# Optimization experiments

Hardware: AMD Instinct MI355X
Metric: run time of the kernel (lower is better)

Reference implementation:

```python
import jax, jax.numpy as jnp
import numpy as np

B, N, D, S, ITERS, EPS = 32, 4096, 512, 8, 3, 1e-8


def layer_norm(x, g, b, eps=1e-5):
    mu = jnp.mean(x, axis=-1, keepdims=True)
    var = jnp.var(x, axis=-1, keepdims=True)
    return (x - mu) * jax.lax.rsqrt(var + eps) * g + b


def setup_inputs() -> dict:
    key = jax.random.key(0)
    ks = jax.random.split(key, 12)
    sc = 1.0 / np.sqrt(D)
    return {
        "inputs": jax.random.normal(ks[0], (B, N, D), jnp.float32),
        "noise": jax.random.normal(ks[1], (B, S, D), jnp.float32),
        "slots_mu": jax.random.normal(ks[2], (1, S, D), jnp.float32),
        "slots_sigma": jnp.ones((1, S, D), jnp.float32),
        "ln_in_g": jnp.ones((D,), jnp.float32), "ln_in_b": jnp.zeros((D,), jnp.float32),
        "ln_s_g": jnp.ones((D,), jnp.float32), "ln_s_b": jnp.zeros((D,), jnp.float32),
        "wq": jax.random.normal(ks[3], (D, D), jnp.float32) * sc,
        "wk": jax.random.normal(ks[4], (D, D), jnp.float32) * sc,
        "wv": jax.random.normal(ks[5], (D, D), jnp.float32) * sc,
        "w_ih": jax.random.normal(ks[6], (3 * D, D), jnp.float32) * sc,
        "w_hh": jax.random.normal(ks[7], (3 * D, D), jnp.float32) * sc,
        "b_ih": jnp.zeros((3 * D,), jnp.float32),
        "b_hh": jnp.zeros((3 * D,), jnp.float32),
        "ln_m_g": jnp.ones((D,), jnp.float32), "ln_m_b": jnp.zeros((D,), jnp.float32),
        "w1": jax.random.normal(ks[8], (D, D), jnp.float32) * sc,
        "b1": jnp.zeros((D,), jnp.float32),
        "w2": jax.random.normal(ks[9], (D, D), jnp.float32) * sc,
        "b2": jnp.zeros((D,), jnp.float32),
    }


def reference(inputs, noise, slots_mu, slots_sigma, ln_in_g, ln_in_b, ln_s_g, ln_s_b,
              wq, wk, wv, w_ih, w_hh, b_ih, b_hh, ln_m_g, ln_m_b, w1, b1, w2, b2):
    # slot init: mu + sigma * N(0,1)
    slots = slots_mu + slots_sigma * noise          # (B,S,D)
    x = layer_norm(inputs, ln_in_g, ln_in_b)        # (B,N,D)
    k = jnp.einsum('bnd,ed->bne', x, wk)            # (B,N,D)
    v = jnp.einsum('bnd,ed->bne', x, wv)            # (B,N,D)
    for _ in range(ITERS):
        slots_prev = slots
        sn = layer_norm(slots, ln_s_g, ln_s_b)
        q = jnp.einsum('bsd,ed->bse', sn, wq)       # (B,S,D)
        logits = jnp.einsum('bnd,bsd->bns', k, q)   # (B,N,S)
        attn = jax.nn.softmax(logits, axis=-1) + EPS  # softmax over slots
        attn = attn / jnp.sum(attn, axis=-1, keepdims=True)
        attn_t = jnp.swapaxes(attn, -1, -2)         # (B,S,N)
        updates = jnp.einsum('bsn,bnd->bsd', attn_t, v)
        # GRUCell(input=updates, hidden=slots_prev)
        gi = jnp.einsum('bsd,ed->bse', updates, w_ih) + b_ih
        gh = jnp.einsum('bsd,ed->bse', slots_prev, w_hh) + b_hh
        gi_r, gi_z, gi_n = jnp.split(gi, 3, axis=-1)
        gh_r, gh_z, gh_n = jnp.split(gh, 3, axis=-1)
        r = jax.nn.sigmoid(gi_r + gh_r)
        z = jax.nn.sigmoid(gi_z + gh_z)
        n = jnp.tanh(gi_n + r * gh_n)
        slots = (1.0 - z) * n + z * slots_prev
        # residual MLP
        h = layer_norm(slots, ln_m_g, ln_m_b)
        h = jax.nn.relu(jnp.einsum('bsd,ed->bse', h, w1) + b1)
        slots = slots + jnp.einsum('bsd,ed->bse', h, w2) + b2
    return slots
```

## Files before the change

kernel.cpp:

```cpp
#include <hip/hip_runtime.h>

#define B_ 32
#define N_ 4096
#define D_ 512
#define S_ 8
#define ITERS_ 3

__device__ __forceinline__ float sigmoid_f(float x) {
    return 1.0f / (1.0f + __expf(-x));
}
__device__ __forceinline__ float tanh_f(float x) {
    float e = __expf(2.0f * x);
    return 1.0f - 2.0f / (e + 1.0f);
}

template<int WT, int LNA>
__device__ void gemm_body(const float* __restrict__ A, const float* __restrict__ W,
                          const float* __restrict__ bias, float* __restrict__ C,
                          int M, int N, int K, int bxi, int byi,
                          const float* __restrict__ stats,
                          const float* __restrict__ lng, const float* __restrict__ lnb,
                          float* smem) {
    float (*As)[68] = (float (*)[68])smem;
    float (*Ws)[36] = (float (*)[36])(smem + 64 * 68);
    int t  = threadIdx.x;
    int bm = byi * 64, bn = bxi * 32;
    int tm = t >> 4, tn = t & 15;
    float acc[4][2] = {{0.f,0.f},{0.f,0.f},{0.f,0.f},{0.f,0.f}};

    for (int kk = 0; kk < K; kk += 64) {
        __syncthreads();
        if (WT == 2) {
#pragma unroll
            for (int r = 0; r < 4; ++r) {
                int idx = t + r * 256;
                int k = idx >> 4, m4 = idx & 15;
                float4 a4 = *(const float4*)(A + (size_t)(kk + k) * M + bm + (m4 << 2));
                *(float4*)&As[k][m4 << 2] = a4;
            }
        } else {
#pragma unroll
            for (int r = 0; r < 4; ++r) {
                int flat = t * 4 + r * 1024;
                int m = flat >> 6, k = flat & 63;
                float4 a4 = *(const float4*)(A + (size_t)(bm + m) * K + kk + k);
                if (LNA) {
                    float mean = stats[(bm + m) * 2];
                    float rs   = stats[(bm + m) * 2 + 1];
                    float4 g4 = *(const float4*)(lng + kk + k);
                    float4 b4 = *(const float4*)(lnb + kk + k);
                    a4.x = fmaf((a4.x - mean) * rs, g4.x, b4.x);
                    a4.y = fmaf((a4.y - mean) * rs, g4.y, b4.y);
                    a4.z = fmaf((a4.z - mean) * rs, g4.z, b4.z);
                    a4.w = fmaf((a4.w - mean) * rs, g4.w, b4.w);
                }
                As[k + 0][m] = a4.x; As[k + 1][m] = a4.y;
                As[k + 2][m] = a4.z; As[k + 3][m] = a4.w;
            }
        }
        if (WT == 1) {
#pragma unroll
            for (int r = 0; r < 2; ++r) {
                int flat = t * 4 + r * 1024;
                int n = flat >> 6, k = flat & 63;
                float4 w4 = *(const float4*)(W + (size_t)(bn + n) * K + kk + k);
                Ws[k + 0][n] = w4.x; Ws[k + 1][n] = w4.y;
                Ws[k + 2][n] = w4.z; Ws[k + 3][n] = w4.w;
            }
        } else {
#pragma unroll
            for (int r = 0; r < 2; ++r) {
                int flat = t * 4 + r * 1024;
                int k = flat >> 5, n = flat & 31;
                float4 w4 = *(const float4*)(W + (size_t)(kk + k) * N + bn + n);
                *(float4*)&Ws[k][n] = w4;
            }
        }
        __syncthreads();
#pragma unroll
        for (int k = 0; k < 64; ++k) {
            float4 a = *(const float4*)&As[k][tm << 2];
            float2 w = *(const float2*)&Ws[k][tn << 1];
            acc[0][0] = fmaf(a.x, w.x, acc[0][0]); acc[0][1] = fmaf(a.x, w.y, acc[0][1]);
            acc[1][0] = fmaf(a.y, w.x, acc[1][0]); acc[1][1] = fmaf(a.y, w.y, acc[1][1]);
            acc[2][0] = fmaf(a.z, w.x, acc[2][0]); acc[2][1] = fmaf(a.z, w.y, acc[2][1]);
            acc[3][0] = fmaf(a.w, w.x, acc[3][0]); acc[3][1] = fmaf(a.w, w.y, acc[3][1]);
        }
    }
#pragma unroll
    for (int i = 0; i < 4; ++i) {
#pragma unroll
        for (int j = 0; j < 2; ++j) {
            int row = bm + (tm << 2) + i;
            int col = bn + (tn << 1) + j;
            float v = acc[i][j];
            if (bias) v += bias[col];
            C[(size_t)row * N + col] = v;
        }
    }
}

__device__ void init_body(const float* __restrict__ noise, const float* __restrict__ mu,
                          const float* __restrict__ sg, float* __restrict__ slots,
                          float* __restrict__ stats, int blk) {
    int wid = threadIdx.x >> 6, lane = threadIdx.x & 63;
    int row = blk * 4 + wid;
    const float4* nz = (const float4*)(noise + (size_t)row * D_);
    const float4* m4 = (const float4*)(mu + (size_t)(row & 7) * D_);
    const float4* s4 = (const float4*)(sg + (size_t)(row & 7) * D_);
    float4 v0 = nz[lane], v1 = nz[64 + lane];
    float4 a0 = m4[lane], a1 = m4[64 + lane];
    float4 c0 = s4[lane], c1 = s4[64 + lane];
    v0.x = fmaf(c0.x, v0.x, a0.x); v0.y = fmaf(c0.y, v0.y, a0.y);
    v0.z = fmaf(c0.z, v0.z, a0.z); v0.w = fmaf(c0.w, v0.w, a0.w);
    v1.x = fmaf(c1.x, v1.x, a1.x); v1.y = fmaf(c1.y, v1.y, a1.y);
    v1.z = fmaf(c1.z, v1.z, a1.z); v1.w = fmaf(c1.w, v1.w, a1.w);
    float4* o4 = (float4*)(slots + (size_t)row * D_);
    o4[lane] = v0; o4[64 + lane] = v1;
    float s1 = v0.x + v0.y + v0.z + v0.w + v1.x + v1.y + v1.z + v1.w;
    float s2 = v0.x*v0.x; s2 = fmaf(v0.y,v0.y,s2); s2 = fmaf(v0.z,v0.z,s2); s2 = fmaf(v0.w,v0.w,s2);
    s2 = fmaf(v1.x,v1.x,s2); s2 = fmaf(v1.y,v1.y,s2); s2 = fmaf(v1.z,v1.z,s2); s2 = fmaf(v1.w,v1.w,s2);
#pragma unroll
    for (int off = 32; off > 0; off >>= 1) {
        s1 += __shfl_xor(s1, off, 64);
        s2 += __shfl_xor(s2, off, 64);
    }
    if (lane == 0) {
        float mean = s1 * (1.0f / D_);
        float var  = s2 * (1.0f / D_) - mean * mean;
        stats[row * 2]     = mean;
        stats[row * 2 + 1] = rsqrtf(var + 1e-5f);
    }
}

__global__ __launch_bounds__(256) void k_pro(const float* __restrict__ wk, const float* __restrict__ wq,
                                             const float* __restrict__ w_ih, const float* __restrict__ wv,
                                             float* __restrict__ Mqk, float* __restrict__ Wiv,
                                             const float* __restrict__ noise, const float* __restrict__ mu,
                                             const float* __restrict__ sg, float* __restrict__ slots,
                                             float* __restrict__ stats) {
    __shared__ float smem[64 * 68 + 64 * 36];
    int blk = blockIdx.x;
    if (blk < 128) {
        gemm_body<2,0>(wk, wq, nullptr, Mqk, 512, 512, 512, blk & 15, blk >> 4,
                       nullptr, nullptr, nullptr, smem);
    } else if (blk < 512) {
        int t2 = blk - 128;
        gemm_body<0,0>(w_ih, wv, nullptr, Wiv, 1536, 512, 512, t2 & 15, t2 >> 4,
                       nullptr, nullptr, nullptr, smem);
    } else {
        init_body(noise, mu, sg, slots, stats, blk - 512);
    }
}

template<int WT, int LNA>
__global__ __launch_bounds__(256) void k_gemm(const float* __restrict__ A, const float* __restrict__ W,
                                              const float* __restrict__ bias, float* __restrict__ C,
                                              int M, int N, int K,
                                              const float* __restrict__ stats,
                                              const float* __restrict__ lng, const float* __restrict__ lnb) {
    __shared__ float smem[64 * 68 + 64 * 36];
    gemm_body<WT,LNA>(A, W, bias, C, M, N, K, blockIdx.x, blockIdx.y, stats, lng, lnb, smem);
}

template<int FIRST>
__global__ __launch_bounds__(512, 2) void k_attn_gh(const float* __restrict__ x,
                                                    const float* __restrict__ qk,
                                                    const float* __restrict__ g,
                                                    const float* __restrict__ bvec,
                                                    float* __restrict__ part,
                                                    float* __restrict__ bsum,
                                                    float2* __restrict__ murs,
                                                    const float* __restrict__ slots,
                                                    const float* __restrict__ w_hh,
                                                    const float* __restrict__ b_hh,
                                                    float* __restrict__ gg) {
    __shared__ float smem[8704];
    const int blk = blockIdx.x;
    const int t = threadIdx.x;

    if (blk >= 512) {
        const int t2 = blk - 512;
        const int ci = t2 % 24, ri = t2 / 24;
        const int bm = ri * 64, bn = ci * 64;
        float (*As)[68] = (float (*)[68])smem;
        float (*Ws)[68] = (float (*)[68])(smem + 64 * 68);
        const int tm = t >> 5, tn = t & 31;
        float acc[4][2] = {{0.f,0.f},{0.f,0.f},{0.f,0.f},{0.f,0.f}};
        for (int kk = 0; kk < 512; kk += 64) {
            __syncthreads();
#pragma unroll
            for (int r = 0; r < 2; ++r) {
                int flat = t * 4 + r * 2048;
                int m = flat >> 6, k = flat & 63;
                float4 a4 = *(const float4*)(slots + (size_t)(bm + m) * 512 + kk + k);
                As[k + 0][m] = a4.x; As[k + 1][m] = a4.y;
                As[k + 2][m] = a4.z; As[k + 3][m] = a4.w;
            }
#pragma unroll
            for (int r = 0; r < 2; ++r) {
                int flat = t * 4 + r * 2048;
                int n = flat >> 6, k = flat & 63;
                float4 w4 = *(const float4*)(w_hh + (size_t)(bn + n) * 512 + kk + k);
                Ws[k + 0][n] = w4.x; Ws[k + 1][n] = w4.y;
                Ws[k + 2][n] = w4.z; Ws[k + 3][n] = w4.w;
            }
            __syncthreads();
#pragma unroll
            for (int k = 0; k < 64; ++k) {
                const float4 a = *(const float4*)&As[k][tm << 2];
                const float2 w = *(const float2*)&Ws[k][tn << 1];
                acc[0][0] = fmaf(a.x, w.x, acc[0][0]); acc[0][1] = fmaf(a.x, w.y, acc[0][1]);
                acc[1][0] = fmaf(a.y, w.x, acc[1][0]); acc[1][1] = fmaf(a.y, w.y, acc[1][1]);
                acc[2][0] = fmaf(a.z, w.x, acc[2][0]); acc[2][1] = fmaf(a.z, w.y, acc[2][1]);
                acc[3][0] = fmaf(a.w, w.x, acc[3][0]); acc[3][1] = fmaf(a.w, w.y, acc[3][1]);
            }
        }
#pragma unroll
        for (int i = 0; i < 4; ++i) {
#pragma unroll
            for (int j = 0; j < 2; ++j) {
                int row = bm + (tm << 2) + i;
                int col = bn + (tn << 1) + j;
                gg[(size_t)row * 3072 + col] = acc[i][j] + b_hh[col];
            }
        }
        return;
    }

    float* qts  = smem;
    float* dds  = smem + 4096;
    float* wls  = smem + 4480;
    float* mur  = smem + 4864;
    float* redA = smem + 5376;
    float* redB = smem + 5392;
    float* c12  = smem + 5408;
    float* u0s  = smem;
    const int nc = blk & 15, b = blk >> 4;
    const int w = t >> 6, lane = t & 63;
    const size_t rowbase = (size_t)b * N_ + (size_t)nc * 256;

    {
        const float4* qk4 = (const float4*)(qk + (size_t)b * 4096);
        const float4* g4 = (const float4*)g;
        const float4* b4 = (const float4*)bvec;
        float c1p[2], c2p[2];
#pragma unroll
        for (int r = 0; r < 2; ++r) {
            int f = t + r * 512;
            float4 v = qk4[f];
            float4 gg4 = g4[f & 127];
            float4 bb = b4[f & 127];
            float4 qv = make_float4(v.x*gg4.x, v.y*gg4.y, v.z*gg4.z, v.w*gg4.w);
            *(float4*)&qts[((f & 127) * 8 + (f >> 7)) * 4] = qv;
            c1p[r] = qv.x + qv.y + qv.z + qv.w;
            c2p[r] = bb.x*v.x + bb.y*v.y + bb.z*v.z + bb.w*v.w;
        }
#pragma unroll
        for (int off = 32; off > 0; off >>= 1) {
#pragma unroll
            for (int r = 0; r < 2; ++r) {
                c1p[r] += __shfl_xor(c1p[r], off, 64);
                c2p[r] += __shfl_xor(c2p[r], off, 64);
            }
        }
        if (lane == 0) {
            redA[w * 2 + 0] = c1p[0]; redA[w * 2 + 1] = c1p[1];
            redB[w * 2 + 0] = c2p[0]; redB[w * 2 + 1] = c2p[1];
        }
    }
    if (!FIRST && t < 256) {
        float2 mm = murs[rowbase + t];
        mur[2 * t] = mm.x; mur[2 * t + 1] = mm.y;
    }
    __syncthreads();
    if (t < 8) {
        int s = t;
        float v1, v2;
        if (s < 4) { v1 = redA[4*s]       + redA[4*s + 2];     v2 = redB[4*s]       + redB[4*s + 2]; }
        else       { v1 = redA[4*(s-4)+1] + redA[4*(s-4)+3];   v2 = redB[4*(s-4)+1] + redB[4*(s-4)+3]; }
        c12[s] = v1; c12[8 + s] = v2;
    }
    __syncthreads();

    float4 qa[8], qb[8];
#pragma unroll
    for (int s = 0; s < 8; ++s) {
        qa[s] = *(const float4*)&qts[(lane * 8 + s) * 4];
        qb[s] = *(const float4*)&qts[((64 + lane) * 8 + s) * 4];
    }
    float c1r[8], c2r[8];
#pragma unroll
    for (int s = 0; s < 8; ++s) { c1r[s] = c12[s]; c2r[s] = c12[8 + s]; }

    const bool hb5 = (lane & 32) != 0, hb4 = (lane & 16) != 0, hb3 = (lane & 8) != 0;
    const float cnorm = 1.0f / (1.0f + 8.0f * 1e-8f);
    const float eadd  = 1e-8f * cnorm;

    float4 acc0[8], acc1[8];
#pragma unroll
    for (int s = 0; s < 8; ++s) {
        acc0[s] = make_float4(0.f, 0.f, 0.f, 0.f);
        acc1[s] = make_float4(0.f, 0.f, 0.f, 0.f);
    }
    float aS8[8] = {0,0,0,0,0,0,0,0}, tS8[8] = {0,0,0,0,0,0,0,0};

    const float4* xg = (const float4*)(x + rowbase * D_);
    float4 cur[8], nxt[8];
    {
        int r0 = w * 4;
#pragma unroll
        for (int i = 0; i < 4; ++i) {
            cur[2*i]   = xg[(size_t)(r0 + i) * 128 + lane];
            cur[2*i+1] = xg[(size_t)(r0 + i) * 128 + 64 + lane];
        }
    }

    for (int jb = 0; jb < 8; ++jb) {
#pragma unroll
        for (int i = 0; i < 4; ++i) {
            float4 xa = cur[2*i], xb = cur[2*i+1];
            float dd[8];
#pragma unroll
            for (int s = 0; s < 8; ++s) {
                float td = xa.x * qa[s].x;
                td = fmaf(xa.y, qa[s].y, td); td = fmaf(xa.z, qa[s].z, td); td = fmaf(xa.w, qa[s].w, td);
                td = fmaf(xb.x, qb[s].x, td); td = fmaf(xb.y, qb[s].y, td);
                td = fmaf(xb.z, qb[s].z, td); td = fmaf(xb.w, qb[s].w, td);
                dd[s] = td;
            }
            float r4[4];
#pragma unroll
            for (int s = 0; s < 4; ++s) {
                float snd = hb5 ? dd[s] : dd[s + 4];
                float kp  = hb5 ? dd[s + 4] : dd[s];
                r4[s] = kp + __shfl_xor(snd, 32, 64);
            }
            float r2v[2];
#pragma unroll
            for (int s = 0; s < 2; ++s) {
                float snd = hb4 ? r4[s] : r4[s + 2];
                float kp  = hb4 ? r4[s + 2] : r4[s];
                r2v[s] = kp + __shfl_xor(snd, 16, 64);
            }
            float v;
            {
                float snd = hb3 ? r2v[0] : r2v[1];
                float kp  = hb3 ? r2v[1] : r2v[0];
                v = kp + __shfl_xor(snd, 8, 64);
            }
            v += __shfl_xor(v, 4, 64);
            v += __shfl_xor(v, 2, 64);
            v += __shfl_xor(v, 1, 64);
            int rb = w * 4 + i;
            if ((lane & 7) == 0) dds[rb * 12 + (lane >> 3)] = v;

            if (FIRST) {
                float sx = xa.x + xa.y + xa.z + xa.w + xb.x + xb.y + xb.z + xb.w;
                float sxx = xa.x*xa.x; sxx = fmaf(xa.y,xa.y,sxx); sxx = fmaf(xa.z,xa.z,sxx); sxx = fmaf(xa.w,xa.w,sxx);
                sxx = fmaf(xb.x,xb.x,sxx); sxx = fmaf(xb.y,xb.y,sxx); sxx = fmaf(xb.z,xb.z,sxx); sxx = fmaf(xb.w,xb.w,sxx);
#pragma unroll
                for (int off = 32; off > 0; off >>= 1) {
                    sx  += __shfl_xor(sx, off, 64);
                    sxx += __shfl_xor(sxx, off, 64);
                }
                float mean = sx * (1.0f / D_);
                float rs   = rsqrtf(sxx * (1.0f / D_) - mean * mean + 1e-5f);
                if (lane == 0) {
                    int br = jb * 32 + rb;
                    mur[br * 2] = mean; mur[br * 2 + 1] = rs;
                    murs[rowbase + br] = make_float2(mean, rs);
                }
            }
        }
        __syncthreads();
        if (w == 0 && lane < 32) {
            int br = jb * 32 + lane;
            float4 d03 = *(const float4*)&dds[lane * 12];
            float4 d47 = *(const float4*)&dds[lane * 12 + 4];
            float mean = mur[br * 2], rs = mur[br * 2 + 1];
            float mc = -rs * mean;
            float lg[8];
            lg[0] = fmaf(rs, d03.x, fmaf(mc, c1r[0], c2r[0]));
            lg[1] = fmaf(rs, d03.y, fmaf(mc, c1r[1], c2r[1]));
            lg[2] = fmaf(rs, d03.z, fmaf(mc, c1r[2], c2r[2]));
            lg[3] = fmaf(rs, d03.w, fmaf(mc, c1r[3], c2r[3]));
            lg[4] = fmaf(rs, d47.x, fmaf(mc, c1r[4], c2r[4]));
            lg[5] = fmaf(rs, d47.y, fmaf(mc, c1r[5], c2r[5]));
            lg[6] = fmaf(rs, d47.z, fmaf(mc, c1r[6], c2r[6]));
            lg[7] = fmaf(rs, d47.w, fmaf(mc, c1r[7], c2r[7]));
            float mx = lg[0];
#pragma unroll
            for (int s = 1; s < 8; ++s) mx = fmaxf(mx, lg[s]);
            float p[8], psum = 0.f;
#pragma unroll
            for (int s = 0; s < 8; ++s) { p[s] = __expf(lg[s] - mx); psum += p[s]; }
            float ip = cnorm / psum;
            float wv[8];
#pragma unroll
            for (int s = 0; s < 8; ++s) {
                float a = fmaf(p[s], ip, eadd);
                wv[s] = a * rs;
                aS8[s] += a;
                tS8[s] = fmaf(wv[s], mean, tS8[s]);
            }
            *(float4*)&wls[lane * 12]     = make_float4(wv[0], wv[1], wv[2], wv[3]);
            *(float4*)&wls[lane * 12 + 4] = make_float4(wv[4], wv[5], wv[6], wv[7]);
        }
        __syncthreads();
        {
            int jn = (jb < 7) ? jb + 1 : 7;
            int r0 = jn * 32 + w * 4;
#pragma unroll
            for (int i = 0; i < 4; ++i) {
                nxt[2*i]   = xg[(size_t)(r0 + i) * 128 + lane];
                nxt[2*i+1] = xg[(size_t)(r0 + i) * 128 + 64 + lane];
            }
        }
#pragma unroll
        for (int i = 0; i < 4; ++i) {
            int rb = w * 4 + i;
            float4 w03 = *(const float4*)&wls[rb * 12];
            float4 w47 = *(const float4*)&wls[rb * 12 + 4];
            float4 xa = cur[2*i], xb = cur[2*i+1];
            acc0[0].x = fmaf(w03.x, xa.x, acc0[0].x); acc0[0].y = fmaf(w03.x, xa.y, acc0[0].y);
            acc0[0].z = fmaf(w03.x, xa.z, acc0[0].z); acc0[0].w = fmaf(w03.x, xa.w, acc0[0].w);
            acc1[0].x = fmaf(w03.x, xb.x, acc1[0].x); acc1[0].y = fmaf(w03.x, xb.y, acc1[0].y);
            acc1[0].z = fmaf(w03.x, xb.z, acc1[0].z); acc1[0].w = fmaf(w03.x, xb.w, acc1[0].w);
            acc0[1].x = fmaf(w03.y, xa.x, acc0[1].x); acc0[1].y = fmaf(w03.y, xa.y, acc0[1].y);
            acc0[1].z = fmaf(w03.y, xa.z, acc0[1].z); acc0[1].w = fmaf(w03.y, xa.w, acc0[1].w);
            acc1[1].x = fmaf(w03.y, xb.x, acc1[1].x); acc1[1].y = fmaf(w03.y, xb.y, acc1[1].y);
            acc1[1].z = fmaf(w03.y, xb.z, acc1[1].z); acc1[1].w = fmaf(w03.y, xb.w, acc1[1].w);
            acc0[2].x = fmaf(w03.z, xa.x, acc0[2].x); acc0[2].y = fmaf(w03.z, xa.y, acc0[2].y);
            acc0[2].z = fmaf(w03.z, xa.z, acc0[2].z); acc0[2].w = fmaf(w03.z, xa.w, acc0[2].w);
            acc1[2].x = fmaf(w03.z, xb.x, acc1[2].x); acc1[2].y = fmaf(w03.z, xb.y, acc1[2].y);
            acc1[2].z = fmaf(w03.z, xb.z, acc1[2].z); acc1[2].w = fmaf(w03.z, xb.w, acc1[2].w);
            acc0[3].x = fmaf(w03.w, xa.x, acc0[3].x); acc0[3].y = fmaf(w03.w, xa.y, acc0[3].y);
            acc0[3].z = fmaf(w03.w, xa.z, acc0[3].z); acc0[3].w = fmaf(w03.w, xa.w, acc0[3].w);
            acc1[3].x = fmaf(w03.w, xb.x, acc1[3].x); acc1[3].y = fmaf(w03.w, xb.y, acc1[3].y);
            acc1[3].z = fmaf(w03.w, xb.z, acc1[3].z); acc1[3].w = fmaf(w03.w, xb.w, acc1[3].w);
            acc0[4].x = fmaf(w47.x, xa.x, acc0[4].x); acc0[4].y = fmaf(w47.x, xa.y, acc0[4].y);
            acc0[4].z = fmaf(w47.x, xa.z, acc0[4].z); acc0[4].w = fmaf(w47.x, xa.w, acc0[4].w);
            acc1[4].x = fmaf(w47.x, xb.x, acc1[4].x); acc1[4].y = fmaf(w47.x, xb.y, acc1[4].y);
            acc1[4].z = fmaf(w47.x, xb.z, acc1[4].z); acc1[4].w = fmaf(w47.x, xb.w, acc1[4].w);
            acc0[5].x = fmaf(w47.y, xa.x, acc0[5].x); acc0[5].y = fmaf(w47.y, xa.y, acc0[5].y);
            acc0[5].z = fmaf(w47.y, xa.z, acc0[5].z); acc0[5].w = fmaf(w47.y, xa.w, acc0[5].w);
            acc1[5].x = fmaf(w47.y, xb.x, acc1[5].x); acc1[5].y = fmaf(w47.y, xb.y, acc1[5].y);
            acc1[5].z = fmaf(w47.y, xb.z, acc1[5].z); acc1[5].w = fmaf(w47.y, xb.w, acc1[5].w);
            acc0[6].x = fmaf(w47.z, xa.x, acc0[6].x); acc0[6].y = fmaf(w47.z, xa.y, acc0[6].y);
            acc0[6].z = fmaf(w47.z, xa.z, acc0[6].z); acc0[6].w = fmaf(w47.z, xa.w, acc0[6].w);
            acc1[6].x = fmaf(w47.z, xb.x, acc1[6].x); acc1[6].y = fmaf(w47.z, xb.y, acc1[6].y);
            acc1[6].z = fmaf(w47.z, xb.z, acc1[6].z); acc1[6].w = fmaf(w47.z, xb.w, acc1[6].w);
            acc0[7].x = fmaf(w47.w, xa.x, acc0[7].x); acc0[7].y = fmaf(w47.w, xa.y, acc0[7].y);
            acc0[7].z = fmaf(w47.w, xa.z, acc0[7].z); acc0[7].w = fmaf(w47.w, xa.w, acc0[7].w);
            acc1[7].x = fmaf(w47.w, xb.x, acc1[7].x); acc1[7].y = fmaf(w47.w, xb.y, acc1[7].y);
            acc1[7].z = fmaf(w47.w, xb.z, acc1[7].z); acc1[7].w = fmaf(w47.w, xb.w, acc1[7].w);
        }
#pragma unroll
        for (int i = 0; i < 8; ++i) cur[i] = nxt[i];
        __syncthreads();
    }

    if (w == 0) {
#pragma unroll
        for (int off = 32; off > 0; off >>= 1) {
#pragma unroll
            for (int s = 0; s < 8; ++s) {
                aS8[s] += __shfl_xor(aS8[s], off, 64);
                tS8[s] += __shfl_xor(tS8[s], off, 64);
            }
        }
        if (lane == 0) {
            float* bs = bsum + (size_t)(b * 16 + nc) * 16;
#pragma unroll
            for (int s = 0; s < 8; ++s) { bs[s] = aS8[s]; bs[8 + s] = tS8[s]; }
        }
    }
    for (int w2 = 0; w2 < 8; ++w2) {
        if (w == w2) {
#pragma unroll
            for (int s = 0; s < 8; ++s) {
                float* p0 = &u0s[s * 512 + (lane << 2)];
                float* p1 = p0 + 256;
                if (w2 == 0) {
                    *(float4*)p0 = acc0[s];
                    *(float4*)p1 = acc1[s];
                } else {
                    float4 v0 = *(float4*)p0;
                    v0.x += acc0[s].x; v0.y += acc0[s].y; v0.z += acc0[s].z; v0.w += acc0[s].w;
                    *(float4*)p0 = v0;
                    float4 v1 = *(float4*)p1;
                    v1.x += acc1[s].x; v1.y += acc1[s].y; v1.z += acc1[s].z; v1.w += acc1[s].w;
                    *(float4*)p1 = v1;
                }
            }
        }
        __syncthreads();
    }
    float4* d4 = (float4*)(part + (size_t)(b * 16 + nc) * 4096);
    const float4* s4 = (const float4*)u0s;
    d4[t] = s4[t];
    d4[t + 512] = s4[t + 512];
}

__global__ __launch_bounds__(512) void k_ured(const float* __restrict__ part,
                                              const float* __restrict__ bsum,
                                              const float* __restrict__ g,
                                              const float* __restrict__ bvec,
                                              float* __restrict__ u0) {
    const int bs = blockIdx.x;
    const int b = bs >> 3, s = bs & 7;
    const int d = threadIdx.x;
    float Av = 0.f, Tv = 0.f;
#pragma unroll
    for (int nc = 0; nc < 16; ++nc) {
        Av += bsum[(size_t)(b * 16 + nc) * 16 + s];
        Tv += bsum[(size_t)(b * 16 + nc) * 16 + 8 + s];
    }
    float p = 0.f;
#pragma unroll
    for (int nc = 0; nc < 16; ++nc)
        p += part[(size_t)(b * 16 + nc) * 4096 + s * 512 + d];
    u0[(size_t)bs * 512 + d] = fmaf(g[d], p - Tv, Av * bvec[d]);
}

__global__ __launch_bounds__(256) void k_gi(const float* __restrict__ u0,
                                            const float* __restrict__ Wiv,
                                            const float* __restrict__ b_ih,
                                            float* __restrict__ gg) {
    __shared__ float As[64][68];
    __shared__ float Ws[64][36];
    const int t = threadIdx.x;
    const int bn = blockIdx.x * 32;
    const int bm = blockIdx.y * 64;
    int tm = t >> 4, tn = t & 15;
    float acc[4][2] = {{0.f,0.f},{0.f,0.f},{0.f,0.f},{0.f,0.f}};

    for (int kk = 0; kk < 512; kk += 64) {
        __syncthreads();
#pragma unroll
        for (int r = 0; r < 4; ++r) {
            int flat = t * 4 + r * 1024;
            int m = flat >> 6, k = flat & 63;
            float4 a4 = *(const float4*)(u0 + (size_t)(bm + m) * 512 + kk + k);
            As[k + 0][m] = a4.x; As[k + 1][m] = a4.y;
            As[k + 2][m] = a4.z; As[k + 3][m] = a4.w;
        }
#pragma unroll
        for (int r = 0; r < 2; ++r) {
            int flat = t * 4 + r * 1024;
            int n = flat >> 6, k = flat & 63;
            float4 w4 = *(const float4*)(Wiv + (size_t)(bn + n) * 512 + kk + k);
            Ws[k + 0][n] = w4.x; Ws[k + 1][n] = w4.y;
            Ws[k + 2][n] = w4.z; Ws[k + 3][n] = w4.w;
        }
        __syncthreads();
#pragma unroll
        for (int k = 0; k < 64; ++k) {
            float4 a = *(const float4*)&As[k][tm << 2];
            float2 w = *(const float2*)&Ws[k][tn << 1];
            acc[0][0] = fmaf(a.x, w.x, acc[0][0]); acc[0][1] = fmaf(a.x, w.y, acc[0][1]);
            acc[1][0] = fmaf(a.y, w.x, acc[1][0]); acc[1][1] = fmaf(a.y, w.y, acc[1][1]);
            acc[2][0] = fmaf(a.z, w.x, acc[2][0]); acc[2][1] = fmaf(a.z, w.y, acc[2][1]);
            acc[3][0] = fmaf(a.w, w.x, acc[3][0]); acc[3][1] = fmaf(a.w, w.y, acc[3][1]);
        }
    }
#pragma unroll
    for (int i = 0; i < 4; ++i) {
#pragma unroll
        for (int j = 0; j < 2; ++j) {
            int row = bm + (tm << 2) + i;
            int cw  = bn + (tn << 1) + j;
            gg[(size_t)row * 3072 + 1536 + cw] = acc[i][j] + b_ih[cw];
        }
    }
}

__global__ __launch_bounds__(512) void k_p2(const float* __restrict__ gg,
                                            const float* __restrict__ slots,
                                            const float* __restrict__ w1, const float* __restrict__ b1,
                                            const float* __restrict__ w2, const float* __restrict__ b2,
                                            const float* __restrict__ wqkT,
                                            const float* __restrict__ ln_m_g, const float* __restrict__ ln_m_b,
                                            const float* __restrict__ ln_s_g, const float* __restrict__ ln_s_b,
                                            float* __restrict__ dst, float* __restrict__ qkout, int last) {
    __shared__ float s2s[2][512];
    __shared__ float t0s[2][512];
    __shared__ float hs[2][512];
    __shared__ float stat[4];
    const int t = threadIdx.x;
    const int wid = t >> 6, lane = t & 63;
    const int r0 = blockIdx.x * 2;

#pragma unroll
    for (int j = 0; j < 2; ++j) {
        int flat = t + j * 512;
        int r = flat >> 9, d = flat & 511;
        size_t row = r0 + r;
        const float* ghb = gg + row * 3072;
        const float* gib = ghb + 1536;
        float gir = gib[d], giz = gib[d + 512], gin = gib[d + 1024];
        float ghr = ghb[d], ghz = ghb[d + 512], ghn = ghb[d + 1024];
        float rr = sigmoid_f(gir + ghr);
        float zz = sigmoid_f(giz + ghz);
        float nn = tanh_f(fmaf(rr, ghn, gin));
        float sp = slots[row * 512 + d];
        s2s[r][d] = fmaf(1.0f - zz, nn, zz * sp);
    }
    __syncthreads();
    if (wid < 2) {
        const float4* sr = (const float4*)s2s[wid];
        float4 a = sr[lane], bq = sr[64 + lane];
        float s1 = a.x + a.y + a.z + a.w + bq.x + bq.y + bq.z + bq.w;
        float s2 = a.x*a.x; s2 = fmaf(a.y,a.y,s2); s2 = fmaf(a.z,a.z,s2); s2 = fmaf(a.w,a.w,s2);
        s2 = fmaf(bq.x,bq.x,s2); s2 = fmaf(bq.y,bq.y,s2); s2 = fmaf(bq.z,bq.z,s2); s2 = fmaf(bq.w,bq.w,s2);
#pragma unroll
        for (int off = 32; off > 0; off >>= 1) {
            s1 += __shfl_xor(s1, off, 64);
            s2 += __shfl_xor(s2, off, 64);
        }
        if (lane == 0) {
            float mean = s1 * (1.0f / D_);
            float var  = s2 * (1.0f / D_) - mean * mean;
            stat[wid * 2] = mean;
            stat[wid * 2 + 1] = rsqrtf(var + 1e-5f);
        }
    }
    __syncthreads();
#pragma unroll
    for (int j = 0; j < 2; ++j) {
        int flat = t + j * 512;
        int r = flat >> 9, d = flat & 511;
        t0s[r][d] = fmaf((s2s[r][d] - stat[r * 2]) * stat[r * 2 + 1], ln_m_g[d], ln_m_b[d]);
    }
    __syncthreads();
    {
        const int c = t;
        const float4* wr = (const float4*)(w1 + (size_t)c * 512);
        float a0 = 0.f, a1 = 0.f;
#pragma unroll 8
        for (int k4 = 0; k4 < 128; ++k4) {
            float4 w4 = wr[k4];
            float4 q0 = *(const float4*)&t0s[0][k4 << 2];
            float4 q1 = *(const float4*)&t0s[1][k4 << 2];
            a0 = fmaf(q0.x, w4.x, a0); a0 = fmaf(q0.y, w4.y, a0);
            a0 = fmaf(q0.z, w4.z, a0); a0 = fmaf(q0.w, w4.w, a0);
            a1 = fmaf(q1.x, w4.x, a1); a1 = fmaf(q1.y, w4.y, a1);
            a1 = fmaf(q1.z, w4.z, a1); a1 = fmaf(q1.w, w4.w, a1);
        }
        float bc = b1[c];
        hs[0][c] = fmaxf(a0 + bc, 0.f);
        hs[1][c] = fmaxf(a1 + bc, 0.f);
    }
    __syncthreads();
    {
        const int c = t;
        const float4* wr = (const float4*)(w2 + (size_t)c * 512);
        float a0 = 0.f, a1 = 0.f;
#pragma unroll 8
        for (int k4 = 0; k4 < 128; ++k4) {
            float4 w4 = wr[k4];
            float4 q0 = *(const float4*)&hs[0][k4 << 2];
            float4 q1 = *(const float4*)&hs[1][k4 << 2];
            a0 = fmaf(q0.x, w4.x, a0); a0 = fmaf(q0.y, w4.y, a0);
            a0 = fmaf(q0.z, w4.z, a0); a0 = fmaf(q0.w, w4.w, a0);
            a1 = fmaf(q1.x, w4.x, a1); a1 = fmaf(q1.y, w4.y, a1);
            a1 = fmaf(q1.z, w4.z, a1); a1 = fmaf(q1.w, w4.w, a1);
        }
        float bc = b2[c];
        float o0 = s2s[0][c] + a0 + bc;
        float o1 = s2s[1][c] + a1 + bc;
        dst[(size_t)r0 * 512 + c] = o0;
        dst[(size_t)(r0 + 1) * 512 + c] = o1;
        s2s[0][c] = o0;
        s2s[1][c] = o1;
    }
    if (last) return;
    __syncthreads();
    if (wid < 2) {
        const float4* sr = (const float4*)s2s[wid];
        float4 a = sr[lane], bq = sr[64 + lane];
        float s1 = a.x + a.y + a.z + a.w + bq.x + bq.y + bq.z + bq.w;
        float s2 = a.x*a.x; s2 = fmaf(a.y,a.y,s2); s2 = fmaf(a.z,a.z,s2); s2 = fmaf(a.w,a.w,s2);
        s2 = fmaf(bq.x,bq.x,s2); s2 = fmaf(bq.y,bq.y,s2); s2 = fmaf(bq.z,bq.z,s2); s2 = fmaf(bq.w,bq.w,s2);
#pragma unroll
        for (int off = 32; off > 0; off >>= 1) {
            s1 += __shfl_xor(s1, off, 64);
            s2 += __shfl_xor(s2, off, 64);
        }
        if (lane == 0) {
            float mean = s1 * (1.0f / D_);
            float var  = s2 * (1.0f / D_) - mean * mean;
            stat[wid * 2] = mean;
            stat[wid * 2 + 1] = rsqrtf(var + 1e-5f);
        }
    }
    __syncthreads();
#pragma unroll
    for (int j = 0; j < 2; ++j) {
        int flat = t + j * 512;
        int r = flat >> 9, d = flat & 511;
        t0s[r][d] = fmaf((s2s[r][d] - stat[r * 2]) * stat[r * 2 + 1], ln_s_g[d], ln_s_b[d]);
    }
    __syncthreads();
    {
        const int c = t;
        const float4* wr = (const float4*)(wqkT + (size_t)c * 512);
        float a0 = 0.f, a1 = 0.f;
#pragma unroll 8
        for (int k4 = 0; k4 < 128; ++k4) {
            float4 w4 = wr[k4];
            float4 q0 = *(const float4*)&t0s[0][k4 << 2];
            float4 q1 = *(const float4*)&t0s[1][k4 << 2];
            a0 = fmaf(q0.x, w4.x, a0); a0 = fmaf(q0.y, w4.y, a0);
            a0 = fmaf(q0.z, w4.z, a0); a0 = fmaf(q0.w, w4.w, a0);
            a1 = fmaf(q1.x, w4.x, a1); a1 = fmaf(q1.y, w4.y, a1);
            a1 = fmaf(q1.z, w4.z, a1); a1 = fmaf(q1.w, w4.w, a1);
        }
        qkout[(size_t)r0 * 512 + c] = a0;
        qkout[(size_t)(r0 + 1) * 512 + c] = a1;
    }
}

extern "C" void kernel_launch(void* const* d_in, const int* in_sizes, int n_in,
                              void* d_out, int out_size, void* d_ws, size_t ws_size,
                              hipStream_t stream) {
    const float* inputs  = (const float*)d_in[0];
    const float* noise   = (const float*)d_in[1];
    const float* mu      = (const float*)d_in[2];
    const float* sg      = (const float*)d_in[3];
    const float* ln_in_g = (const float*)d_in[4];
    const float* ln_in_b = (const float*)d_in[5];
    const float* ln_s_g  = (const float*)d_in[6];
    const float* ln_s_b  = (const float*)d_in[7];
    const float* wq      = (const float*)d_in[8];
    const float* wk      = (const float*)d_in[9];
    const float* wv      = (const float*)d_in[10];
    const float* w_ih    = (const float*)d_in[11];
    const float* w_hh    = (const float*)d_in[12];
    const float* b_ih    = (const float*)d_in[13];
    const float* b_hh    = (const float*)d_in[14];
    const float* ln_m_g  = (const float*)d_in[15];
    const float* ln_m_b  = (const float*)d_in[16];
    const float* w1      = (const float*)d_in[17];
    const float* b1      = (const float*)d_in[18];
    const float* w2      = (const float*)d_in[19];
    const float* b2      = (const float*)d_in[20];

    float* ws = (float*)d_ws;
    const size_t SLOT = (size_t)B_ * S_ * D_;
    size_t o = 0;
    float* slots = ws + o; o += SLOT;
    float* qk    = ws + o; o += SLOT;
    float* u0    = ws + o; o += SLOT;
    float* gg    = ws + o; o += (size_t)256 * 3072;
    float* Mqk   = ws + o; o += (size_t)D_ * D_;
    float* Wiv   = ws + o; o += (size_t)3 * D_ * D_;
    float* statsS= ws + o; o += 512;
    float* part  = ws + o; o += (size_t)16 * B_ * 4096;
    float* bsum  = ws + o; o += (size_t)B_ * 16 * 16;
    float2* murs = (float2*)(ws + o); o += (size_t)2 * B_ * N_;

    k_pro<<<576, 256, 0, stream>>>(wk, wq, w_ih, wv, Mqk, Wiv, noise, mu, sg, slots, statsS);
    k_gemm<1,1><<<dim3(16, 4), 256, 0, stream>>>(slots, Mqk, nullptr, qk,
                                                 256, 512, 512, statsS, ln_s_g, ln_s_b);

    for (int it = 0; it < ITERS_; ++it) {
        if (it == 0)
            k_attn_gh<1><<<608, 512, 0, stream>>>(inputs, qk, ln_in_g, ln_in_b, part, bsum,
                                                  murs, slots, w_hh, b_hh, gg);
        else
            k_attn_gh<0><<<608, 512, 0, stream>>>(inputs, qk, ln_in_g, ln_in_b, part, bsum,
                                                  murs, slots, w_hh, b_hh, gg);
        k_ured<<<256, 512, 0, stream>>>(part, bsum, ln_in_g, ln_in_b, u0);
        k_gi<<<dim3(48, 4), 256, 0, stream>>>(u0, Wiv, b_ih, gg);
        int last = (it == ITERS_ - 1);
        float* dst = last ? (float*)d_out : slots;
        k_p2<<<128, 512, 0, stream>>>(gg, slots, w1, b1, w2, b2, Mqk,
                                      ln_m_g, ln_m_b, ln_s_g, ln_s_b, dst, qk, last);
    }
}
```

Before: 693.6 us.

## Relax attn kernel occupancy, swizzle q smem layout, schedule gh GEMM blocks first

Changes the attention+GRU-hidden kernel's launch bounds from 2 to 1 blocks per CU to allow more registers. It also moves the 96 w_hh GEMM blocks to the front of the grid so they are scheduled before the 512 attention blocks. It XOR-swizzles the q tile layout in shared memory to avoid LDS bank conflicts on the per-lane float4 reads. It reads the c1/c2 constants from shared memory at use instead of holding them in registers. Together these aim to cut register pressure and spills, plus bank conflicts, at the cost of lower occupancy and less latency hiding.

Result: faster. 677.0 us (-2.4%).

```diff
diff --git a/kernel.cpp b/kernel.cpp
--- a/kernel.cpp
+++ b/kernel.cpp
@@ -164,7 +164,7 @@
 }
 
 template<int FIRST>
-__global__ __launch_bounds__(512, 2) void k_attn_gh(const float* __restrict__ x,
+__global__ __launch_bounds__(512, 1) void k_attn_gh(const float* __restrict__ x,
                                                     const float* __restrict__ qk,
                                                     const float* __restrict__ g,
                                                     const float* __restrict__ bvec,
@@ -179,9 +179,8 @@
     const int blk = blockIdx.x;
     const int t = threadIdx.x;
 
-    if (blk >= 512) {
-        const int t2 = blk - 512;
-        const int ci = t2 % 24, ri = t2 / 24;
+    if (blk < 96) {
+        const int ci = blk % 24, ri = blk / 24;
         const int bm = ri * 64, bn = ci * 64;
         float (*As)[68] = (float (*)[68])smem;
         float (*Ws)[68] = (float (*)[68])(smem + 64 * 68);
@@ -236,7 +235,8 @@
     float* redB = smem + 5392;
     float* c12  = smem + 5408;
     float* u0s  = smem;
-    const int nc = blk & 15, b = blk >> 4;
+    const int ablk = blk - 96;
+    const int nc = ablk & 15, b = ablk >> 4;
     const int w = t >> 6, lane = t & 63;
     const size_t rowbase = (size_t)b * N_ + (size_t)nc * 256;
 
@@ -248,11 +248,12 @@
 #pragma unroll
         for (int r = 0; r < 2; ++r) {
             int f = t + r * 512;
+            int k4 = f & 127, sidx = f >> 7;
             float4 v = qk4[f];
-            float4 gg4 = g4[f & 127];
-            float4 bb = b4[f & 127];
+            float4 gg4 = g4[k4];
+            float4 bb = b4[k4];
             float4 qv = make_float4(v.x*gg4.x, v.y*gg4.y, v.z*gg4.z, v.w*gg4.w);
-            *(float4*)&qts[((f & 127) * 8 + (f >> 7)) * 4] = qv;
+            *(float4*)&qts[(k4 * 8 + (sidx ^ (k4 & 7))) * 4] = qv;
             c1p[r] = qv.x + qv.y + qv.z + qv.w;
             c2p[r] = bb.x*v.x + bb.y*v.y + bb.z*v.z + bb.w*v.w;
         }
@@ -286,12 +287,9 @@
     float4 qa[8], qb[8];
 #pragma unroll
     for (int s = 0; s < 8; ++s) {
-        qa[s] = *(const float4*)&qts[(lane * 8 + s) * 4];
-        qb[s] = *(const float4*)&qts[((64 + lane) * 8 + s) * 4];
-    }
-    float c1r[8], c2r[8];
-#pragma unroll
-    for (int s = 0; s < 8; ++s) { c1r[s] = c12[s]; c2r[s] = c12[8 + s]; }
+        qa[s] = *(const float4*)&qts[(lane * 8 + (s ^ (lane & 7))) * 4];
+        qb[s] = *(const float4*)&qts[((64 + lane) * 8 + (s ^ (lane & 7))) * 4];
+    }
 
     const bool hb5 = (lane & 32) != 0, hb4 = (lane & 16) != 0, hb3 = (lane & 8) != 0;
     const float cnorm = 1.0f / (1.0f + 8.0f * 1e-8f);
@@ -381,14 +379,14 @@
             float mean = mur[br * 2], rs = mur[br * 2 + 1];
             float mc = -rs * mean;
             float lg[8];
-            lg[0] = fmaf(rs, d03.x, fmaf(mc, c1r[0], c2r[0]));
-            lg[1] = fmaf(rs, d03.y, fmaf(mc, c1r[1], c2r[1]));
-            lg[2] = fmaf(rs, d03.z, fmaf(mc, c1r[2], c2r[2]));
-            lg[3] = fmaf(rs, d03.w, fmaf(mc, c1r[3], c2r[3]));
-            lg[4] = fmaf(rs, d47.x, fmaf(mc, c1r[4], c2r[4]));
-            lg[5] = fmaf(rs, d47.y, fmaf(mc, c1r[5], c2r[5]));
-            lg[6] = fmaf(rs, d47.z, fmaf(mc, c1r[6], c2r[6]));
-            lg[7] = fmaf(rs, d47.w, fmaf(mc, c1r[7], c2r[7]));
+            lg[0] = fmaf(rs, d03.x, fmaf(mc, c12[0], c12[8]));
+            lg[1] = fmaf(rs, d03.y, fmaf(mc, c12[1], c12[9]));
+            lg[2] = fmaf(rs, d03.z, fmaf(mc, c12[2], c12[10]));
+            lg[3] = fmaf(rs, d03.w, fmaf(mc, c12[3], c12[11]));
+            lg[4] = fmaf(rs, d47.x, fmaf(mc, c12[4], c12[12]));
+            lg[5] = fmaf(rs, d47.y, fmaf(mc, c12[5], c12[13]));
+            lg[6] = fmaf(rs, d47.z, fmaf(mc, c12[6], c12[14]));
+            lg[7] = fmaf(rs, d47.w, fmaf(mc, c12[7], c12[15]));
             float mx = lg[0];
 #pragma unroll
             for (int s = 1; s < 8; ++s) mx = fmaxf(mx, lg[s]);
```
